# Performance work log

Measured on AMD Instinct MI355X. Metric: run time of the kernel, lower is better.

## Reference

```python
import jax, jax.numpy as jnp
import numpy as np

B, V, C, H, W = 2, 4, 64, 256, 256
RADIUS = 2.0
R = 2  # integer splat footprint half-width = ceil(RADIUS)
EPS = 1e-8
FOCAL = 256.0


def _rt(tx, ty, tz):
    M = np.eye(4, dtype=np.float32)
    M[0, 3], M[1, 3], M[2, 3] = tx, ty, tz
    return M


def setup_inputs() -> dict:
    key = jax.random.key(0)
    k1, k2 = jax.random.split(key)
    feats = jax.random.normal(k1, (B, V, C, H, W), dtype=jnp.float32)
    # depths in [1, 5): positive, realistic metric range
    depths = 1.0 + 4.0 * jax.random.uniform(k2, (B, V, 1, H, W), dtype=jnp.float32)
    Km = np.eye(4, dtype=np.float32)
    Km[0, 0] = FOCAL; Km[1, 1] = FOCAL
    Km[0, 2] = W / 2.0; Km[1, 2] = H / 2.0
    K = jnp.asarray(np.tile(Km[None], (B, 1, 1)))
    src = np.stack([_rt(0.05 * v, 0.0, 0.0) for v in range(V)], 0)  # (V,4,4)
    src_RTs = jnp.asarray(np.tile(src[None], (B, 1, 1, 1)))
    src_RTinvs = jnp.linalg.inv(src_RTs)
    dst = _rt(0.02, 0.0, 0.1)
    dst_RTs = jnp.asarray(np.tile(dst[None, None], (B, 1, 1, 1)))
    dst_RTinvs = jnp.linalg.inv(dst_RTs)
    return {"feats": feats, "depths": depths, "K": K, "src_RTs": src_RTs,
            "src_RTinvs": src_RTinvs, "dst_RTs": dst_RTs, "dst_RTinvs": dst_RTinvs}


def _project_and_splat(feats, depths, K, src_RTinvs, dst_RTs):
    Bn, Vn, Cn, Hn, Wn = feats.shape
    N = Hn * Wn
    BV = Bn * Vn
    # pixel grid (homogeneous image coords), row-major so flat idx = y*W + x
    xs = jnp.arange(Wn, dtype=feats.dtype)
    ys = jnp.arange(Hn, dtype=feats.dtype)
    gx, gy = jnp.meshgrid(xs, ys, indexing="xy")  # (H,W)
    gx = gx.reshape(-1); gy = gy.reshape(-1)      # (N,)
    d = depths.reshape(Bn, Vn, 1, N)
    ones = jnp.ones_like(d)
    # view_to_world_coord: [x*d, y*d, d, 1] -> K^-1 -> RTinv
    proj = jnp.concatenate([gx * d, gy * d, d, ones], axis=2)  # (B,V,4,N)
    Kinv = jnp.linalg.inv(K)
    cam = jnp.einsum("bij,bvjn->bvin", Kinv, proj)
    world = jnp.einsum("bvij,bvjn->bvin", src_RTinvs, cam)
    # world_to_view: dst RT -> K -> perspective divide
    cam2 = jnp.einsum("bij,bvjn->bvin", dst_RTs.reshape(Bn, 4, 4), world)
    xyp = jnp.einsum("bij,bvjn->bvin", K, cam2)
    z = xyp[:, :, 2].reshape(BV, N)
    x = (xyp[:, :, 0] / (xyp[:, :, 2] + EPS)).reshape(BV, N)
    y = (xyp[:, :, 1] / (xyp[:, :, 2] + EPS)).reshape(BV, N)
    # radius splatting: scatter-accumulate over a (2R+1)^2 footprint,
    # linear falloff in pixel distance, soft z-buffer via 1/z weighting
    fN = feats.reshape(BV, Cn, N).transpose(0, 2, 1)  # (BV,N,C)
    acc = jnp.zeros((BV * N, Cn), feats.dtype)
    wz = jnp.zeros((BV * N, 2), feats.dtype)  # [:,0]=sum w, [:,1]=sum w*z
    boff = (jnp.arange(BV) * N)[:, None]
    px0 = jnp.round(x); py0 = jnp.round(y)
    invz = 1.0 / (z + EPS)
    for dy in range(-R, R + 1):
        for dx in range(-R, R + 1):
            px = px0 + dx; py = py0 + dy
            dist = jnp.sqrt((px - x) ** 2 + (py - y) ** 2 + EPS)
            w = jnp.maximum(0.0, 1.0 - dist / RADIUS)
            valid = (px >= 0) & (px < Wn) & (py >= 0) & (py < Hn) & (z > EPS)
            w = jnp.where(valid, w * invz, 0.0)
            ix = jnp.clip(px.astype(jnp.int32), 0, Wn - 1)
            iy = jnp.clip(py.astype(jnp.int32), 0, Hn - 1)
            idx = (boff + iy * Wn + ix).reshape(-1)
            acc = acc.at[idx].add((w[..., None] * fN).reshape(-1, Cn))
            wz = wz.at[idx].add(jnp.stack([w, w * z], -1).reshape(-1, 2))
    wsum = wz[:, 0:1]; zsum = wz[:, 1:2]
    prj_feats = (acc / (wsum + EPS)).reshape(Bn, Vn, Hn, Wn, Cn).transpose(0, 1, 4, 2, 3)
    prj_depth = (zsum / (wsum + EPS)).reshape(Bn, Vn, Hn, Wn, 1).transpose(0, 1, 4, 2, 3)
    return jnp.concatenate([prj_feats, prj_depth], axis=2)  # (B,V,C+1,H,W)


def reference(feats, depths, K, src_RTs, src_RTinvs, dst_RTs, dst_RTinvs):
    return _project_and_splat(feats, depths, K, src_RTinvs, dst_RTs)
```

## Files before the change

kernel.cpp:

```cpp
#include <hip/hip_runtime.h>

#define Wd 256
#define Hd 256
#define Nn 65536
#define Cc 64
#define Vv 4
#define Bb 2
#define BVn 8
#define EPSf 1e-8f

#define OFF_COUNT   ((size_t)0)
#define OFF_OFFS    ((size_t)2  << 20)
#define OFF_CURS    ((size_t)4  << 20)
#define OFF_ROWSUM  ((size_t)6  << 20)
#define OFF_ROWBASE (((size_t)6 << 20) + 65536)
#define OFF_STAGE1  ((size_t)8  << 20)
#define OFF_BINNED  ((size_t)16 << 20)
#define OFF_FT      ((size_t)24 << 20)
#define FT_BYTES    ((size_t)BVn * Nn * Cc * 4)
#define NEED_FULL   (OFF_FT + FT_BYTES)
#define NEED_MID    OFF_FT

__device__ inline void mat4_mul(const float* A, const float* B, float* C) {
#pragma unroll
  for (int i = 0; i < 4; i++)
#pragma unroll
    for (int j = 0; j < 4; j++) {
      float s = 0.f;
#pragma unroll
      for (int k = 0; k < 4; k++) s += A[i * 4 + k] * B[k * 4 + j];
      C[i * 4 + j] = s;
    }
}

__device__ inline void mat4_inv(const float* m, float* invOut) {
  float inv[16];
  inv[0] = m[5]*m[10]*m[15] - m[5]*m[11]*m[14] - m[9]*m[6]*m[15] +
           m[9]*m[7]*m[14] + m[13]*m[6]*m[11] - m[13]*m[7]*m[10];
  inv[4] = -m[4]*m[10]*m[15] + m[4]*m[11]*m[14] + m[8]*m[6]*m[15] -
           m[8]*m[7]*m[14] - m[12]*m[6]*m[11] + m[12]*m[7]*m[10];
  inv[8] = m[4]*m[9]*m[15] - m[4]*m[11]*m[13] - m[8]*m[5]*m[15] +
           m[8]*m[7]*m[13] + m[12]*m[5]*m[11] - m[12]*m[7]*m[9];
  inv[12] = -m[4]*m[9]*m[14] + m[4]*m[10]*m[13] + m[8]*m[5]*m[14] -
            m[8]*m[6]*m[13] - m[12]*m[5]*m[10] + m[12]*m[6]*m[9];
  inv[1] = -m[1]*m[10]*m[15] + m[1]*m[11]*m[14] + m[9]*m[2]*m[15] -
           m[9]*m[3]*m[14] - m[13]*m[2]*m[11] + m[13]*m[3]*m[10];
  inv[5] = m[0]*m[10]*m[15] - m[0]*m[11]*m[14] - m[8]*m[2]*m[15] +
           m[8]*m[3]*m[14] + m[12]*m[2]*m[11] - m[12]*m[3]*m[10];
  inv[9] = -m[0]*m[9]*m[15] + m[0]*m[11]*m[13] + m[8]*m[1]*m[15] -
           m[8]*m[3]*m[13] - m[12]*m[1]*m[11] + m[12]*m[3]*m[9];
  inv[13] = m[0]*m[9]*m[14] - m[0]*m[10]*m[13] - m[8]*m[1]*m[14] +
            m[8]*m[2]*m[13] + m[12]*m[1]*m[10] - m[12]*m[2]*m[9];
  inv[2] = m[1]*m[6]*m[15] - m[1]*m[7]*m[14] - m[5]*m[2]*m[15] +
           m[5]*m[3]*m[14] + m[13]*m[2]*m[7] - m[13]*m[3]*m[6];
  inv[6] = -m[0]*m[6]*m[15] + m[0]*m[7]*m[14] + m[4]*m[2]*m[15] -
           m[4]*m[3]*m[14] - m[12]*m[2]*m[7] + m[12]*m[3]*m[6];
  inv[10] = m[0]*m[5]*m[15] - m[0]*m[7]*m[13] - m[4]*m[1]*m[15] +
            m[4]*m[3]*m[13] + m[12]*m[1]*m[7] - m[12]*m[3]*m[5];
  inv[14] = -m[0]*m[5]*m[14] + m[0]*m[6]*m[13] + m[4]*m[1]*m[14] -
            m[4]*m[2]*m[13] - m[12]*m[1]*m[6] + m[12]*m[2]*m[5];
  inv[3] = -m[1]*m[6]*m[11] + m[1]*m[7]*m[10] + m[5]*m[2]*m[11] -
           m[5]*m[3]*m[10] - m[9]*m[2]*m[7] + m[9]*m[3]*m[6];
  inv[7] = m[0]*m[6]*m[11] - m[0]*m[7]*m[10] - m[4]*m[2]*m[11] +
           m[4]*m[3]*m[10] + m[8]*m[2]*m[7] - m[8]*m[3]*m[6];
  inv[11] = -m[0]*m[5]*m[11] + m[0]*m[7]*m[9] + m[4]*m[1]*m[11] -
            m[4]*m[3]*m[9] - m[8]*m[1]*m[7] + m[8]*m[3]*m[5];
  inv[15] = m[0]*m[5]*m[10] - m[0]*m[6]*m[9] - m[4]*m[1]*m[10] +
            m[4]*m[2]*m[9] + m[8]*m[1]*m[6] - m[8]*m[2]*m[5];
  float det = m[0]*inv[0] + m[1]*inv[4] + m[2]*inv[8] + m[3]*inv[12];
  det = 1.0f / det;
#pragma unroll
  for (int i = 0; i < 16; i++) invOut[i] = inv[i] * det;
}

__device__ inline void compute_T(const float* Kmat, const float* srcinv,
                                 const float* dstRT, int b, int bv, float* T) {
  float Kinv[16], M1[16], M2[16];
  mat4_inv(Kmat + b * 16, Kinv);
  mat4_mul(srcinv + bv * 16, Kinv, M1);
  mat4_mul(dstRT + b * 16, M1, M2);
  mat4_mul(Kmat + b * 16, M2, T);
}

__global__ __launch_bounds__(256) void transpose_kernel(
    const float* __restrict__ feats, float* __restrict__ featsT) {
  __shared__ float lds[Cc][65];
  const int bv = blockIdx.x >> 10;
  const int n0 = (blockIdx.x & 1023) << 6;
  const int t = threadIdx.x;

  const float* src = feats + (size_t)bv * Cc * Nn;
  {
    const int c_l = t >> 6;
    const int n_l = t & 63;
#pragma unroll
    for (int i = 0; i < 16; i++) {
      const int c = c_l * 16 + i;
      lds[c][n_l] = src[(size_t)c * Nn + n0 + n_l];
    }
  }
  __syncthreads();
  {
    const int c_l = t & 63;
    const int n_b = t >> 6;
    float* dst = featsT + ((size_t)bv * Nn + n0) * Cc;
#pragma unroll
    for (int i = 0; i < 16; i++) {
      const int n = n_b * 16 + i;
      dst[(size_t)n * Cc + c_l] = lds[c_l][n];
    }
  }
}

__global__ __launch_bounds__(256) void project_count_kernel(
    const float* __restrict__ depths, const float* __restrict__ Kmat,
    const float* __restrict__ srcinv, const float* __restrict__ dstRT,
    unsigned int* __restrict__ counts, float4* __restrict__ stage1) {
  const int bv = blockIdx.x >> 8;
  const int n = ((blockIdx.x & 255) << 8) | threadIdx.x;
  const int b = bv >> 2;

  __shared__ float T[16];
  if (threadIdx.x == 0) compute_T(Kmat, srcinv, dstRT, b, bv, T);
  __syncthreads();

  const float d = depths[(size_t)bv * Nn + n];
  const float gx = (float)(n & (Wd - 1));
  const float gy = (float)(n >> 8);

  const float p0 = (T[0] * gx + T[1] * gy + T[2]) * d + T[3];
  const float p1 = (T[4] * gx + T[5] * gy + T[6]) * d + T[7];
  const float z  = (T[8] * gx + T[9] * gy + T[10]) * d + T[11];

  const float ze = z + EPSf;
  const float x = p0 / ze;
  const float y = p1 / ze;
  const float px0 = rintf(x);
  const float py0 = rintf(y);

  int bin = -1;
  if (z > EPSf && px0 >= -2.0f && px0 <= (float)(Wd + 1) &&
      py0 >= -2.0f && py0 <= (float)(Hd + 1)) {
    const int bx = min(max((int)px0, 0), Wd - 1);
    const int by = min(max((int)py0, 0), Hd - 1);
    bin = (bv << 16) | (by << 8) | bx;
    atomicAdd(&counts[bin], 1u);
  }
  float4 rec;
  rec.x = x; rec.y = y; rec.z = z; rec.w = __int_as_float(bin);
  stage1[(size_t)bv * Nn + n] = rec;
}

__global__ __launch_bounds__(256) void row_sum_kernel(
    const unsigned int* __restrict__ counts, unsigned int* __restrict__ rowsum) {
  const int r = blockIdx.x * 256 + threadIdx.x;
  unsigned int s = 0;
  const unsigned int* c = counts + (size_t)r * 256;
  for (int i = 0; i < 256; i++) s += c[i];
  rowsum[r] = s;
}

__global__ __launch_bounds__(256) void scan_rows_kernel(
    const unsigned int* __restrict__ rowsum, unsigned int* __restrict__ rowbase) {
  __shared__ unsigned int part[256];
  const int t = threadIdx.x;
  unsigned int loc[8];
  unsigned int run = 0;
#pragma unroll
  for (int i = 0; i < 8; i++) {
    loc[i] = run;
    run += rowsum[t * 8 + i];
  }
  part[t] = run;
  __syncthreads();
  for (int off = 1; off < 256; off <<= 1) {
    unsigned int x = part[t];
    unsigned int y = (t >= off) ? part[t - off] : 0u;
    __syncthreads();
    part[t] = x + y;
    __syncthreads();
  }
  const unsigned int base = (t == 0) ? 0u : part[t - 1];
#pragma unroll
  for (int i = 0; i < 8; i++) rowbase[t * 8 + i] = base + loc[i];
}

__global__ __launch_bounds__(256) void bin_offsets_kernel(
    const unsigned int* __restrict__ counts, const unsigned int* __restrict__ rowbase,
    unsigned int* __restrict__ offs, unsigned int* __restrict__ curs) {
  const int r = blockIdx.x * 256 + threadIdx.x;
  unsigned int run = rowbase[r];
  const size_t base = (size_t)r * 256;
  for (int i = 0; i < 256; i++) {
    const unsigned int c = counts[base + i];
    offs[base + i] = run;
    curs[base + i] = run;
    run += c;
  }
}

__global__ __launch_bounds__(256) void fill_kernel(
    const float4* __restrict__ stage1, unsigned int* __restrict__ curs,
    float4* __restrict__ binned) {
  const int g = blockIdx.x * 256 + threadIdx.x;
  float4 rec = stage1[g];
  const int bin = __float_as_int(rec.w);
  if (bin >= 0) {
    const unsigned int slot = atomicAdd(&curs[bin], 1u);
    rec.w = __int_as_float(g & (Nn - 1));
    binned[slot] = rec;
  }
}

template <bool TRANS>
__global__ __launch_bounds__(256) void gather_kernel(
    const float* __restrict__ featsAny,
    const unsigned int* __restrict__ offs, const unsigned int* __restrict__ curs,
    const float4* __restrict__ binned, float* __restrict__ out) {
  const int bv = blockIdx.x >> 8;
  const int vrow = blockIdx.x & 255;
  const int u = threadIdx.x;

  float acc[Cc];
#pragma unroll
  for (int c = 0; c < Cc; c++) acc[c] = 0.f;
  float wsum = 0.f, wz = 0.f;

  const float uf = (float)u, vf = (float)vrow;
  const int by_lo = max(0, vrow - 2), by_hi = min(Hd - 1, vrow + 2);
  const int bx_lo = max(0, u - 2), bx_hi = min(Wd - 1, u + 2);

  for (int by = by_lo; by <= by_hi; by++) {
    const int rowb = (bv << 16) | (by << 8);
    const unsigned int s = offs[rowb + bx_lo];
    const unsigned int e = curs[rowb + bx_hi];
    for (unsigned int r = s; r < e; r++) {
      const float4 rec = binned[r];
      const float ddx = uf - rec.x;
      const float ddy = vf - rec.y;
      const float dist = sqrtf(ddx * ddx + ddy * ddy + EPSf);
      float w = 1.0f - dist * 0.5f;
      if (w > 0.f) {
        w *= 1.0f / (rec.z + EPSf);
        wsum += w;
        wz += w * rec.z;
        const int n = __float_as_int(rec.w);
        if (TRANS) {
          const float4* fs = reinterpret_cast<const float4*>(
              featsAny + ((size_t)(bv << 16 | n)) * Cc);
#pragma unroll
          for (int i = 0; i < 16; i++) {
            const float4 fv = fs[i];
            acc[4 * i + 0] += w * fv.x;
            acc[4 * i + 1] += w * fv.y;
            acc[4 * i + 2] += w * fv.z;
            acc[4 * i + 3] += w * fv.w;
          }
        } else {
          const float* fp = featsAny + ((size_t)bv * Cc << 16) + n;
#pragma unroll
          for (int c = 0; c < Cc; c++) acc[c] += w * fp[(size_t)c << 16];
        }
      }
    }
  }

  const float inv = 1.0f / (wsum + EPSf);
  const int dest = (vrow << 8) | u;
  float* ob = out + (((size_t)bv * 65) << 16) + dest;
#pragma unroll
  for (int c = 0; c < Cc; c++) ob[(size_t)c << 16] = acc[c] * inv;
  ob[(size_t)Cc << 16] = wz * inv;
}

__global__ __launch_bounds__(256) void splat_kernel(
    const float* __restrict__ feats, const float* __restrict__ depths,
    const float* __restrict__ Kmat, const float* __restrict__ srcinv,
    const float* __restrict__ dstRT, float* __restrict__ out,
    float* __restrict__ wsum) {
  const int bv = blockIdx.x >> 8;
  const int n = ((blockIdx.x & 255) << 8) | threadIdx.x;
  const int b = bv >> 2;

  __shared__ float T[16];
  if (threadIdx.x == 0) compute_T(Kmat, srcinv, dstRT, b, bv, T);
  __syncthreads();

  const float d = depths[(size_t)bv * Nn + n];
  const float gx = (float)(n & (Wd - 1));
  const float gy = (float)(n >> 8);
  const float p0 = (T[0] * gx + T[1] * gy + T[2]) * d + T[3];
  const float p1 = (T[4] * gx + T[5] * gy + T[6]) * d + T[7];
  const float z  = (T[8] * gx + T[9] * gy + T[10]) * d + T[11];
  const float ze = z + EPSf;
  const float x = p0 / ze, y = p1 / ze;
  const float zi = 1.0f / ze;
  const float px0 = rintf(x), py0 = rintf(y);
  const bool zok = (z > EPSf);

  float f[Cc];
  const float* fp = feats + (size_t)bv * Cc * Nn + n;
#pragma unroll
  for (int c = 0; c < Cc; c++) f[c] = fp[(size_t)c * Nn];

  float* outbv = out + (size_t)bv * 65 * Nn;
  float* wbv = wsum + (size_t)bv * Nn;
#pragma unroll
  for (int dy = -2; dy <= 2; dy++) {
#pragma unroll
    for (int dx = -2; dx <= 2; dx++) {
      const float px = px0 + (float)dx;
      const float py = py0 + (float)dy;
      const float ddx = px - x, ddy = py - y;
      const float dist = sqrtf(ddx * ddx + ddy * ddy + EPSf);
      float w = fmaxf(0.0f, 1.0f - dist * 0.5f);
      const bool valid = zok && (px >= 0.0f) && (px < (float)Wd) &&
                         (py >= 0.0f) && (py < (float)Hd);
      w = valid ? w * zi : 0.0f;
      if (w > 0.0f) {
        const int idx = (int)py * Wd + (int)px;
        atomicAdd(wbv + idx, w);
        atomicAdd(outbv + (size_t)Cc * Nn + idx, w * z);
#pragma unroll
        for (int c = 0; c < Cc; c++)
          atomicAdd(outbv + (size_t)c * Nn + idx, w * f[c]);
      }
    }
  }
}

__global__ __launch_bounds__(256) void norm_kernel(float* __restrict__ out,
                                                   const float* __restrict__ wsum) {
  const int t = blockIdx.x * 256 + threadIdx.x;
  const int n = t & 0xFFFF;
  const int bvc = t >> 16;
  const int bv = bvc / 65;
  const float wv = wsum[(size_t)bv * Nn + n];
  out[t] = out[t] / (wv + EPSf);
}

extern "C" void kernel_launch(void* const* d_in, const int* in_sizes, int n_in,
                              void* d_out, int out_size, void* d_ws, size_t ws_size,
                              hipStream_t stream) {
  const float* feats  = (const float*)d_in[0];
  const float* depths = (const float*)d_in[1];
  const float* Kmat   = (const float*)d_in[2];
  const float* srcinv = (const float*)d_in[4];
  const float* dstRT  = (const float*)d_in[5];
  float* out = (float*)d_out;
  char* ws = (char*)d_ws;

  if (ws_size >= NEED_MID) {
    unsigned int* counts = (unsigned int*)(ws + OFF_COUNT);
    unsigned int* offs   = (unsigned int*)(ws + OFF_OFFS);
    unsigned int* curs   = (unsigned int*)(ws + OFF_CURS);
    unsigned int* rowsum = (unsigned int*)(ws + OFF_ROWSUM);
    unsigned int* rowbase= (unsigned int*)(ws + OFF_ROWBASE);
    float4* stage1 = (float4*)(ws + OFF_STAGE1);
    float4* binned = (float4*)(ws + OFF_BINNED);
    float* featsT  = (float*)(ws + OFF_FT);

    hipMemsetAsync(counts, 0, (size_t)BVn * Nn * sizeof(unsigned int), stream);

    const bool trans = (ws_size >= NEED_FULL);
    if (trans)
      transpose_kernel<<<dim3(BVn * (Nn / 64)), dim3(256), 0, stream>>>(feats, featsT);

    project_count_kernel<<<dim3(BVn * (Nn / 256)), dim3(256), 0, stream>>>(
        depths, Kmat, srcinv, dstRT, counts, stage1);
    row_sum_kernel<<<dim3(8), dim3(256), 0, stream>>>(counts, rowsum);
    scan_rows_kernel<<<dim3(1), dim3(256), 0, stream>>>(rowsum, rowbase);
    bin_offsets_kernel<<<dim3(8), dim3(256), 0, stream>>>(counts, rowbase, offs, curs);
    fill_kernel<<<dim3(BVn * Nn / 256), dim3(256), 0, stream>>>(stage1, curs, binned);

    if (trans)
      gather_kernel<true><<<dim3(BVn * Hd), dim3(256), 0, stream>>>(
          featsT, offs, curs, binned, out);
    else
      gather_kernel<false><<<dim3(BVn * Hd), dim3(256), 0, stream>>>(
          feats, offs, curs, binned, out);
  } else {
    float* wsum = (float*)ws;
    hipMemsetAsync(out, 0, (size_t)out_size * sizeof(float), stream);
    hipMemsetAsync(wsum, 0, (size_t)BVn * Nn * sizeof(float), stream);
    splat_kernel<<<dim3(BVn * (Nn / 256)), dim3(256), 0, stream>>>(
        feats, depths, Kmat, srcinv, dstRT, out, wsum);
    norm_kernel<<<dim3(BVn * 65 * Nn / 256), dim3(256), 0, stream>>>(out, wsum);
  }
}
```

Before: 614.0 us.

## Stage features in bin order during fill and split gather over channel groups

The separate transpose kernel is removed. The fill kernel now scatters each point's 64 features into a bin-ordered buffer, together with a precomputed 1/z, so the gather reads features contiguously in the same order it walks the bins. The gather kernel is split into 4 channel groups of 16, which cuts per-thread accumulator registers and quadruples the block count. The row-sum and bin-offset kernels move from one serial loop per thread to wavefront shuffle reductions and scans across many more blocks. In exchange, fill does strided uncoalesced feature reads, and gather repeats the record walk and weight computation once per channel group.

```diff
diff --git a/kernel.cpp b/kernel.cpp
--- a/kernel.cpp
+++ b/kernel.cpp
@@ -82,36 +82,6 @@
   mat4_mul(Kmat + b * 16, M2, T);
 }
 
-__global__ __launch_bounds__(256) void transpose_kernel(
-    const float* __restrict__ feats, float* __restrict__ featsT) {
-  __shared__ float lds[Cc][65];
-  const int bv = blockIdx.x >> 10;
-  const int n0 = (blockIdx.x & 1023) << 6;
-  const int t = threadIdx.x;
-
-  const float* src = feats + (size_t)bv * Cc * Nn;
-  {
-    const int c_l = t >> 6;
-    const int n_l = t & 63;
-#pragma unroll
-    for (int i = 0; i < 16; i++) {
-      const int c = c_l * 16 + i;
-      lds[c][n_l] = src[(size_t)c * Nn + n0 + n_l];
-    }
-  }
-  __syncthreads();
-  {
-    const int c_l = t & 63;
-    const int n_b = t >> 6;
-    float* dst = featsT + ((size_t)bv * Nn + n0) * Cc;
-#pragma unroll
-    for (int i = 0; i < 16; i++) {
-      const int n = n_b * 16 + i;
-      dst[(size_t)n * Cc + c_l] = lds[c_l][n];
-    }
-  }
-}
-
 __global__ __launch_bounds__(256) void project_count_kernel(
     const float* __restrict__ depths, const float* __restrict__ Kmat,
     const float* __restrict__ srcinv, const float* __restrict__ dstRT,
@@ -153,11 +123,14 @@
 
 __global__ __launch_bounds__(256) void row_sum_kernel(
     const unsigned int* __restrict__ counts, unsigned int* __restrict__ rowsum) {
-  const int r = blockIdx.x * 256 + threadIdx.x;
-  unsigned int s = 0;
-  const unsigned int* c = counts + (size_t)r * 256;
-  for (int i = 0; i < 256; i++) s += c[i];
-  rowsum[r] = s;
+  const int wid = threadIdx.x >> 6;
+  const int lane = threadIdx.x & 63;
+  const int r = blockIdx.x * 4 + wid;
+  const uint4 c = reinterpret_cast<const uint4*>(counts + (size_t)r * 256)[lane];
+  unsigned int s = c.x + c.y + c.z + c.w;
+#pragma unroll
+  for (int off = 32; off > 0; off >>= 1) s += __shfl_down(s, off, 64);
+  if (lane == 0) rowsum[r] = s;
 }
 
 __global__ __launch_bounds__(256) void scan_rows_kernel(
@@ -188,42 +161,78 @@
 __global__ __launch_bounds__(256) void bin_offsets_kernel(
     const unsigned int* __restrict__ counts, const unsigned int* __restrict__ rowbase,
     unsigned int* __restrict__ offs, unsigned int* __restrict__ curs) {
-  const int r = blockIdx.x * 256 + threadIdx.x;
-  unsigned int run = rowbase[r];
-  const size_t base = (size_t)r * 256;
-  for (int i = 0; i < 256; i++) {
-    const unsigned int c = counts[base + i];
-    offs[base + i] = run;
-    curs[base + i] = run;
-    run += c;
-  }
-}
-
+  const int wid = threadIdx.x >> 6;
+  const int lane = threadIdx.x & 63;
+  const int r = blockIdx.x * 4 + wid;
+  const uint4 c = reinterpret_cast<const uint4*>(counts + (size_t)r * 256)[lane];
+  const unsigned int t0 = c.x;
+  const unsigned int t1 = t0 + c.y;
+  const unsigned int t2 = t1 + c.z;
+  const unsigned int t3 = t2 + c.w;
+  unsigned int inc = t3;
+#pragma unroll
+  for (int off = 1; off < 64; off <<= 1) {
+    const unsigned int v = __shfl_up(inc, off, 64);
+    if (lane >= off) inc += v;
+  }
+  const unsigned int base = rowbase[r] + inc - t3;
+  uint4 o;
+  o.x = base;
+  o.y = base + t0;
+  o.z = base + t1;
+  o.w = base + t2;
+  reinterpret_cast<uint4*>(offs + (size_t)r * 256)[lane] = o;
+  reinterpret_cast<uint4*>(curs + (size_t)r * 256)[lane] = o;
+}
+
+template <bool FSTAGED>
 __global__ __launch_bounds__(256) void fill_kernel(
-    const float4* __restrict__ stage1, unsigned int* __restrict__ curs,
-    float4* __restrict__ binned) {
+    const float* __restrict__ feats, const float4* __restrict__ stage1,
+    unsigned int* __restrict__ curs, float4* __restrict__ binned,
+    float4* __restrict__ binnedF) {
   const int g = blockIdx.x * 256 + threadIdx.x;
   float4 rec = stage1[g];
   const int bin = __float_as_int(rec.w);
   if (bin >= 0) {
     const unsigned int slot = atomicAdd(&curs[bin], 1u);
-    rec.w = __int_as_float(g & (Nn - 1));
-    binned[slot] = rec;
-  }
-}
-
-template <bool TRANS>
+    const int n = g & (Nn - 1);
+    if (FSTAGED) {
+      rec.w = 1.0f / (rec.z + EPSf);
+      binned[slot] = rec;
+      const int bv = g >> 16;
+      const float* fp = feats + ((size_t)bv * Cc << 16) + n;
+      float4* dst = binnedF + ((size_t)slot << 4);
+#pragma unroll
+      for (int i = 0; i < 16; i++) {
+        float4 v;
+        v.x = fp[(size_t)(4 * i + 0) << 16];
+        v.y = fp[(size_t)(4 * i + 1) << 16];
+        v.z = fp[(size_t)(4 * i + 2) << 16];
+        v.w = fp[(size_t)(4 * i + 3) << 16];
+        dst[i] = v;
+      }
+    } else {
+      rec.w = __int_as_float(n);
+      binned[slot] = rec;
+    }
+  }
+}
+
+template <bool FSTAGED>
 __global__ __launch_bounds__(256) void gather_kernel(
-    const float* __restrict__ featsAny,
+    const float* __restrict__ feats,
     const unsigned int* __restrict__ offs, const unsigned int* __restrict__ curs,
-    const float4* __restrict__ binned, float* __restrict__ out) {
-  const int bv = blockIdx.x >> 8;
-  const int vrow = blockIdx.x & 255;
+    const float4* __restrict__ binned, const float4* __restrict__ binnedF,
+    float* __restrict__ out) {
+  const int bid = blockIdx.x;
+  const int bv = bid >> 10;
+  const int cg = (bid >> 8) & 3;
+  const int vrow = bid & 255;
   const int u = threadIdx.x;
 
-  float acc[Cc];
-#pragma unroll
-  for (int c = 0; c < Cc; c++) acc[c] = 0.f;
+  float acc[16];
+#pragma unroll
+  for (int c = 0; c < 16; c++) acc[c] = 0.f;
   float wsum = 0.f, wz = 0.f;
 
   const float uf = (float)u, vf = (float)vrow;
@@ -239,27 +248,34 @@
       const float ddx = uf - rec.x;
       const float ddy = vf - rec.y;
       const float dist = sqrtf(ddx * ddx + ddy * ddy + EPSf);
-      float w = 1.0f - dist * 0.5f;
-      if (w > 0.f) {
-        w *= 1.0f / (rec.z + EPSf);
+      if (FSTAGED) {
+        const float w = fmaxf(0.0f, 1.0f - dist * 0.5f) * rec.w;
         wsum += w;
         wz += w * rec.z;
-        const int n = __float_as_int(rec.w);
-        if (TRANS) {
-          const float4* fs = reinterpret_cast<const float4*>(
-              featsAny + ((size_t)(bv << 16 | n)) * Cc);
-#pragma unroll
-          for (int i = 0; i < 16; i++) {
-            const float4 fv = fs[i];
-            acc[4 * i + 0] += w * fv.x;
-            acc[4 * i + 1] += w * fv.y;
-            acc[4 * i + 2] += w * fv.z;
-            acc[4 * i + 3] += w * fv.w;
-          }
-        } else {
-          const float* fp = featsAny + ((size_t)bv * Cc << 16) + n;
-#pragma unroll
-          for (int c = 0; c < Cc; c++) acc[c] += w * fp[(size_t)c << 16];
+        const float4* fs = binnedF + ((size_t)r << 4) + (cg << 2);
+        const float4 f0 = fs[0];
+        const float4 f1 = fs[1];
+        const float4 f2 = fs[2];
+        const float4 f3 = fs[3];
+        acc[0]  += w * f0.x; acc[1]  += w * f0.y;
+        acc[2]  += w * f0.z; acc[3]  += w * f0.w;
+        acc[4]  += w * f1.x; acc[5]  += w * f1.y;
+        acc[6]  += w * f1.z; acc[7]  += w * f1.w;
+        acc[8]  += w * f2.x; acc[9]  += w * f2.y;
+        acc[10] += w * f2.z; acc[11] += w * f2.w;
+        acc[12] += w * f3.x; acc[13] += w * f3.y;
+        acc[14] += w * f3.z; acc[15] += w * f3.w;
+      } else {
+        float w = 1.0f - dist * 0.5f;
+        if (w > 0.f) {
+          w *= 1.0f / (rec.z + EPSf);
+          wsum += w;
+          wz += w * rec.z;
+          const int n = __float_as_int(rec.w);
+          const float* fp = feats + ((size_t)bv * Cc << 16) + n;
+#pragma unroll
+          for (int c = 0; c < 16; c++)
+            acc[c] += w * fp[(size_t)(cg * 16 + c) << 16];
         }
       }
     }
@@ -267,10 +283,12 @@
 
   const float inv = 1.0f / (wsum + EPSf);
   const int dest = (vrow << 8) | u;
-  float* ob = out + (((size_t)bv * 65) << 16) + dest;
-#pragma unroll
-  for (int c = 0; c < Cc; c++) ob[(size_t)c << 16] = acc[c] * inv;
-  ob[(size_t)Cc << 16] = wz * inv;
+  float* ob = out + (((size_t)bv * 65) << 16) + ((size_t)(cg * 16) << 16) + dest;
+#pragma unroll
+  for (int c = 0; c < 16; c++) ob[(size_t)c << 16] = acc[c] * inv;
+  if (cg == 0) {
+    out[(((size_t)bv * 65 + Cc) << 16) + dest] = wz * inv;
+  }
 }
 
 __global__ __launch_bounds__(256) void splat_kernel(
@@ -358,27 +376,29 @@
     unsigned int* rowbase= (unsigned int*)(ws + OFF_ROWBASE);
     float4* stage1 = (float4*)(ws + OFF_STAGE1);
     float4* binned = (float4*)(ws + OFF_BINNED);
-    float* featsT  = (float*)(ws + OFF_FT);
+    float4* binnedF= (float4*)(ws + OFF_FT);
 
     hipMemsetAsync(counts, 0, (size_t)BVn * Nn * sizeof(unsigned int), stream);
 
-    const bool trans = (ws_size >= NEED_FULL);
-    if (trans)
-      transpose_kernel<<<dim3(BVn * (Nn / 64)), dim3(256), 0, stream>>>(feats, featsT);
+    const bool staged = (ws_size >= NEED_FULL);
 
     project_count_kernel<<<dim3(BVn * (Nn / 256)), dim3(256), 0, stream>>>(
         depths, Kmat, srcinv, dstRT, counts, stage1);
-    row_sum_kernel<<<dim3(8), dim3(256), 0, stream>>>(counts, rowsum);
+    row_sum_kernel<<<dim3(512), dim3(256), 0, stream>>>(counts, rowsum);
     scan_rows_kernel<<<dim3(1), dim3(256), 0, stream>>>(rowsum, rowbase);
-    bin_offsets_kernel<<<dim3(8), dim3(256), 0, stream>>>(counts, rowbase, offs, curs);
-    fill_kernel<<<dim3(BVn * Nn / 256), dim3(256), 0, stream>>>(stage1, curs, binned);
-
-    if (trans)
-      gather_kernel<true><<<dim3(BVn * Hd), dim3(256), 0, stream>>>(
-          featsT, offs, curs, binned, out);
-    else
-      gather_kernel<false><<<dim3(BVn * Hd), dim3(256), 0, stream>>>(
-          feats, offs, curs, binned, out);
+    bin_offsets_kernel<<<dim3(512), dim3(256), 0, stream>>>(counts, rowbase, offs, curs);
+
+    if (staged) {
+      fill_kernel<true><<<dim3(BVn * Nn / 256), dim3(256), 0, stream>>>(
+          feats, stage1, curs, binned, binnedF);
+      gather_kernel<true><<<dim3(BVn * 4 * Hd), dim3(256), 0, stream>>>(
+          feats, offs, curs, binned, binnedF, out);
+    } else {
+      fill_kernel<false><<<dim3(BVn * Nn / 256), dim3(256), 0, stream>>>(
+          feats, stage1, curs, binned, binnedF);
+      gather_kernel<false><<<dim3(BVn * 4 * Hd), dim3(256), 0, stream>>>(
+          feats, offs, curs, binned, binnedF, out);
+    }
   } else {
     float* wsum = (float*)ws;
     hipMemsetAsync(out, 0, (size_t)out_size * sizeof(float), stream);
```

Result: slower. 717.4 us (+16.8%).
